# Optimization experiments

Hardware: AMD Instinct MI355X
Metric: run time of the kernel (lower is better)

Reference implementation:

```python
import jax, jax.numpy as jnp
import numpy as np

LOOPS = 2
NUM_GROUPS = 4
EXPERTS_PER_GROUP = 2
NUM_EXPERTS = NUM_GROUPS * EXPERTS_PER_GROUP
GROUPS_TOP_K = 2
TOP_K = 1
RMS_EPS = 1e-6
EPS = 1e-9


def setup_inputs() -> dict:
    key = jax.random.key(0)
    ks = jax.random.split(key, 6)
    B, S, D, F = 2, 1024, 1024, 2048
    return {
        "z": jax.random.normal(ks[0], (B, S, D), jnp.float32),
        "norm_w": jnp.ones((D,), jnp.float32),
        "w_macro": jax.random.normal(ks[1], (NUM_GROUPS, D), jnp.float32) * (D ** -0.5),
        "w_micro": jax.random.normal(ks[2], (NUM_GROUPS, EXPERTS_PER_GROUP, D), jnp.float32) * (D ** -0.5),
        "w1": jax.random.normal(ks[3], (NUM_EXPERTS, F, D), jnp.float32) * (D ** -0.5),
        "w2": jax.random.normal(ks[4], (NUM_EXPERTS, D, F), jnp.float32) * (F ** -0.5),
    }


def _rmsnorm(x, w):
    return x * jax.lax.rsqrt(jnp.mean(x * x, axis=-1, keepdims=True) + RMS_EPS) * w


def _combine_weights(x_flat, w_macro, w_micro):
    """Dense [T, E] combine matrix equivalent to the sort-based dispatch."""
    T = x_flat.shape[0]
    macro = jax.nn.softmax(x_flat @ w_macro.T, axis=-1)                    # [T, G]
    mvals, midx = jax.lax.top_k(macro, GROUPS_TOP_K)                       # [T, Gk]
    mvals = mvals / (jnp.sum(mvals, axis=-1, keepdims=True) + EPS)
    micro = jax.nn.softmax(jnp.einsum('td,ged->tge', x_flat, w_micro), axis=-1)  # [T, G, Eg]
    uvals, uidx = jax.lax.top_k(micro, TOP_K)                              # [T, G, k]
    uvals = uvals / (jnp.sum(uvals, axis=-1, keepdims=True) + EPS)
    tok = jnp.arange(T)
    combine = jnp.zeros((T, NUM_EXPERTS), x_flat.dtype)
    for s in range(GROUPS_TOP_K):
        g = midx[:, s]                                                     # [T]
        wg = mvals[:, s:s + 1]                                             # [T, 1]
        li = uidx[tok, g]                                                  # [T, k] local expert ids in group g
        lv = uvals[tok, g]                                                 # [T, k]
        eidx = g[:, None] * EXPERTS_PER_GROUP + li                         # [T, k] global expert ids
        combine = combine.at[tok[:, None], eidx].add(lv * wg)
    return combine


def reference(z, norm_w, w_macro, w_micro, w1, w2):
    B, S, D = z.shape
    T = B * S
    for _ in range(LOOPS):
        zn = _rmsnorm(z, norm_w)
        x = zn.reshape(T, D)
        combine = _combine_weights(x, w_macro, w_micro)                    # [T, E]
        # Dense equivalent of gather -> per-expert FFN -> weighted index_add
        h = jax.nn.silu(jnp.einsum('td,efd->tef', x, w1))                  # [T, E, F]
        y = jnp.einsum('tef,edf->ted', h, w2)                              # [T, E, D]
        mixed = jnp.einsum('ted,te->td', y, combine)                       # [T, D]
        z = z + mixed.reshape(B, S, D)
    return z
```

## Files before the change

kernel.cpp:

```cpp
#include <hip/hip_runtime.h>
#include <cstdint>
#include <cstddef>

#define T_TOK 2048
#define DDIM  1024
#define FDIM  2048

typedef __attribute__((ext_vector_type(8))) short bf16x8;
typedef __attribute__((ext_vector_type(4))) float f32x4;

static __device__ __forceinline__ float b2f(unsigned short u) {
  union { unsigned int i; float f; } v; v.i = ((unsigned int)u) << 16; return v.f;
}
static __device__ __forceinline__ unsigned short f2b(float f) {
  unsigned int x = __float_as_uint(f);
  return (unsigned short)((x + 0x7fffu + ((x >> 16) & 1u)) >> 16);
}
static __device__ __forceinline__ unsigned int pack2(float a, float b) {
  return (unsigned int)f2b(a) | ((unsigned int)f2b(b) << 16);
}
static __device__ __forceinline__ void gload_lds16(const void* g, void* l) {
  __builtin_amdgcn_global_load_lds(
      (const __attribute__((address_space(1))) void*)g,
      (__attribute__((address_space(3))) void*)l, 16, 0, 0);
}

__global__ void k_probe(const unsigned int* __restrict__ nw, int* __restrict__ flag) {
  if (threadIdx.x == 0) flag[0] = (nw[0] == 0x3F800000u) ? 0 : 1;
}

__global__ void k_init(const void* __restrict__ zin, float* __restrict__ z32,
                       const int* __restrict__ flag) {
  const int i = blockIdx.x * blockDim.x + threadIdx.x;
  float4 f;
  if (flag[0]) {
    ushort4 u = ((const ushort4*)zin)[i];
    f.x = b2f(u.x); f.y = b2f(u.y); f.z = b2f(u.z); f.w = b2f(u.w);
  } else {
    f = ((const float4*)zin)[i];
  }
  ((float4*)z32)[i] = f;
}

__global__ void k_out(const float* __restrict__ z32, void* __restrict__ out,
                      const int* __restrict__ flag) {
  const int i = blockIdx.x * blockDim.x + threadIdx.x;
  const float4 a = ((const float4*)z32)[i];
  if (flag[0]) {
    ushort4 o; o.x = f2b(a.x); o.y = f2b(a.y); o.z = f2b(a.z); o.w = f2b(a.w);
    ((ushort4*)out)[i] = o;
  } else {
    ((float4*)out)[i] = a;
  }
}

__global__ void k_split(const float* __restrict__ w, unsigned short* __restrict__ hi,
                        unsigned short* __restrict__ lo, const int* __restrict__ flag) {
  if (flag[0]) return;
  const size_t i = (size_t)blockIdx.x * blockDim.x + threadIdx.x;
  const float4 v = ((const float4*)w)[i];
  ushort4 h, l;
  h.x = f2b(v.x); l.x = f2b(v.x - b2f(h.x));
  h.y = f2b(v.y); l.y = f2b(v.y - b2f(h.y));
  h.z = f2b(v.z); l.z = f2b(v.z - b2f(h.z));
  h.w = f2b(v.w); l.w = f2b(v.w - b2f(h.w));
  ((ushort4*)hi)[i] = h;
  ((ushort4*)lo)[i] = l;
}

__global__ void k_rms_route(const float* __restrict__ z32,
                            const void* __restrict__ nw,
                            const void* __restrict__ wmac,
                            const void* __restrict__ wmic,
                            const int* __restrict__ flag,
                            unsigned short* __restrict__ xh,
                            unsigned short* __restrict__ xl,
                            float* __restrict__ logits,
                            const int base)
{
  const int tl = blockIdx.x;
  const int t  = base + tl;
  const int tid = threadIdx.x;
  const int lane = tid & 63, wv = tid >> 6;
  const int isbf = flag[0];
  const float4 zv = ((const float4*)(z32 + (size_t)t * DDIM))[tid];
  float ss = zv.x*zv.x + zv.y*zv.y + zv.z*zv.z + zv.w*zv.w;
  #pragma unroll
  for (int o = 32; o > 0; o >>= 1) ss += __shfl_down(ss, o);
  __shared__ float red[4];
  __shared__ float lred[12][4];
  if (lane == 0) red[wv] = ss;
  __syncthreads();
  const float tot = red[0] + red[1] + red[2] + red[3];
  const float scale = 1.f / sqrtf(tot * (1.f / DDIM) + 1e-6f);
  float4 nwv;
  if (isbf) {
    ushort4 u = ((const ushort4*)nw)[tid];
    nwv.x = b2f(u.x); nwv.y = b2f(u.y); nwv.z = b2f(u.z); nwv.w = b2f(u.w);
  } else {
    nwv = ((const float4*)nw)[tid];
  }
  float4 xn;
  xn.x = zv.x * scale * nwv.x;
  xn.y = zv.y * scale * nwv.y;
  xn.z = zv.z * scale * nwv.z;
  xn.w = zv.w * scale * nwv.w;
  ushort4 h4, l4;
  h4.x = f2b(xn.x); l4.x = f2b(xn.x - b2f(h4.x));
  h4.y = f2b(xn.y); l4.y = f2b(xn.y - b2f(h4.y));
  h4.z = f2b(xn.z); l4.z = f2b(xn.z - b2f(h4.z));
  h4.w = f2b(xn.w); l4.w = f2b(xn.w - b2f(h4.w));
  ((ushort4*)(xh + (size_t)tl * DDIM))[tid] = h4;
  ((ushort4*)(xl + (size_t)tl * DDIM))[tid] = l4;

  float part[12];
  #pragma unroll
  for (int r = 0; r < 4; r++) {
    float4 w;
    if (isbf) {
      ushort4 u = ((const ushort4*)wmac)[r * 256 + tid];
      w.x = b2f(u.x); w.y = b2f(u.y); w.z = b2f(u.z); w.w = b2f(u.w);
    } else {
      w = ((const float4*)wmac)[r * 256 + tid];
    }
    part[r] = xn.x*w.x + xn.y*w.y + xn.z*w.z + xn.w*w.w;
  }
  #pragma unroll
  for (int r = 0; r < 8; r++) {
    float4 w;
    if (isbf) {
      ushort4 u = ((const ushort4*)wmic)[r * 256 + tid];
      w.x = b2f(u.x); w.y = b2f(u.y); w.z = b2f(u.z); w.w = b2f(u.w);
    } else {
      w = ((const float4*)wmic)[r * 256 + tid];
    }
    part[4 + r] = xn.x*w.x + xn.y*w.y + xn.z*w.z + xn.w*w.w;
  }
  #pragma unroll
  for (int r = 0; r < 12; r++) {
    float v = part[r];
    #pragma unroll
    for (int o = 32; o > 0; o >>= 1) v += __shfl_down(v, o);
    if (lane == 0) lred[r][wv] = v;
  }
  __syncthreads();
  if (tid < 12)
    logits[tl * 12 + tid] = lred[tid][0] + lred[tid][1] + lred[tid][2] + lred[tid][3];
}

__global__ void k_route_a(const float* __restrict__ logits, int* __restrict__ eidx,
                          float* __restrict__ cw, int* __restrict__ counts, const int Tc)
{
  const int t = blockIdx.x * 256 + threadIdx.x;
  if (t >= Tc) return;
  const float* lg = logits + t * 12;
  float p[4];
  float m = fmaxf(fmaxf(lg[0], lg[1]), fmaxf(lg[2], lg[3]));
  float s = 0.f;
  #pragma unroll
  for (int i = 0; i < 4; i++) { p[i] = expf(lg[i] - m); s += p[i]; }
  #pragma unroll
  for (int i = 0; i < 4; i++) p[i] /= s;
  int i1 = 0;
  #pragma unroll
  for (int i = 1; i < 4; i++) if (p[i] > p[i1]) i1 = i;
  int i2 = (i1 == 0) ? 1 : 0;
  #pragma unroll
  for (int i = 0; i < 4; i++) if (i != i1 && p[i] > p[i2]) i2 = i;
  const float denom = p[i1] + p[i2] + 1e-9f;
  const int gs[2] = { i1, i2 };
  #pragma unroll
  for (int sI = 0; sI < 2; sI++) {
    const int g = gs[sI];
    const float wg = p[g] / denom;
    const float u0 = lg[4 + 2*g], u1 = lg[4 + 2*g + 1];
    const int li = (u1 > u0) ? 1 : 0;
    const float uval = 1.f / (1.f + expf(-fabsf(u0 - u1)));
    const float lv = uval / (uval + 1e-9f);
    const int e = g * 2 + li;
    eidx[t*2 + sI] = e;
    cw[t*2 + sI] = wg * lv;
    atomicAdd(&counts[e], 1);
  }
}

__global__ void k_route_b(const int* __restrict__ counts, int* __restrict__ offsets) {
  if (threadIdx.x == 0) {
    int o = 0;
    for (int e = 0; e < 8; e++) { offsets[e] = o; o += counts[e]; }
    offsets[8] = o;
  }
}

__global__ void k_route_c(const int* __restrict__ eidx, const float* __restrict__ cw,
                          const int* __restrict__ offsets, int* __restrict__ counts2,
                          int* __restrict__ tok, float* __restrict__ wof, const int Tc)
{
  const int t = blockIdx.x * 256 + threadIdx.x;
  if (t >= Tc) return;
  #pragma unroll
  for (int sI = 0; sI < 2; sI++) {
    const int e = eidx[t*2 + sI];
    const int pos = atomicAdd(&counts2[e], 1);
    const int a = offsets[e] + pos;
    tok[a] = t;
    wof[a] = cw[t*2 + sI];
  }
}

template<int KDIM, bool IS_G1, int KSPLIT>
__launch_bounds__(256)
__global__ void k_gemm(const unsigned short* __restrict__ Ah,
                       const unsigned short* __restrict__ Al,
                       const void* __restrict__ Bw,
                       const unsigned short* __restrict__ Bh_pre,
                       const unsigned short* __restrict__ Bl_pre,
                       const int* __restrict__ flag,
                       const int presplit,
                       const int* __restrict__ offsets,
                       const int* __restrict__ tok_of_a,
                       const float* __restrict__ w_of_a,
                       unsigned short* __restrict__ hh_out,
                       unsigned short* __restrict__ hl_out,
                       float* __restrict__ z32,
                       const int Nsize, const int base)
{
  const int e = blockIdx.z / KSPLIT;
  const int kpart = blockIdx.z - e * KSPLIT;
  const int offs = offsets[e];
  const int n_e = offsets[e + 1] - offs;
  const int rbase = blockIdx.y * 128;
  if (rbase >= n_e) return;
  const int cbase = blockIdx.x * 128;
  const int isbf = flag[0];

  __shared__ __align__(16) unsigned short Ahs[128 * 64];
  __shared__ __align__(16) unsigned short Als[128 * 64];
  __shared__ __align__(16) unsigned short Bhs[128 * 64];
  __shared__ __align__(16) unsigned short Bls[128 * 64];

  const int tid = threadIdx.x;
  const int lane = tid & 63;
  const int wv = tid >> 6;
  const int wr = (wv >> 1) * 64;
  const int wc = (wv & 1) * 64;
  const int lr = lane & 15;
  const int quad = lane >> 4;

  size_t aoff[4], boff[4];
  int gsw[4], loff[4];
  const int ch = tid & 7;
  #pragma unroll
  for (int c = 0; c < 4; c++) {
    const int row = c * 32 + (tid >> 3);
    int rl = rbase + row; if (rl > n_e - 1) rl = n_e - 1;
    if constexpr (IS_G1) aoff[c] = (size_t)tok_of_a[offs + rl] * KDIM;
    else                 aoff[c] = (size_t)(offs + rl) * KDIM;
    boff[c] = ((size_t)e * Nsize + cbase + row) * (size_t)KDIM;
    gsw[c]  = (ch ^ (row & 7)) * 8;
    loff[c] = row * 64 + gsw[c];
  }
  int lbase[4];
  #pragma unroll
  for (int c = 0; c < 4; c++) lbase[c] = (c * 32 + wv * 8) * 64;

  f32x4 acc[4][4];
  #pragma unroll
  for (int mt = 0; mt < 4; mt++)
    #pragma unroll
    for (int nt = 0; nt < 4; nt++)
      acc[mt][nt] = (f32x4){0.f, 0.f, 0.f, 0.f};

  const int KCH = KDIM / KSPLIT;
  const int k_lo = kpart * KCH;
  for (int k0 = k_lo; k0 < k_lo + KCH; k0 += 64) {
    __syncthreads();
    #pragma unroll
    for (int c = 0; c < 4; c++) {
      gload_lds16(Ah + aoff[c] + k0 + gsw[c], &Ahs[lbase[c]]);
      gload_lds16(Al + aoff[c] + k0 + gsw[c], &Als[lbase[c]]);
    }
    if (isbf) {
      const unsigned short* B16 = (const unsigned short*)Bw;
      #pragma unroll
      for (int c = 0; c < 4; c++)
        gload_lds16(B16 + boff[c] + k0 + gsw[c], &Bhs[lbase[c]]);
    } else if (presplit) {
      #pragma unroll
      for (int c = 0; c < 4; c++) {
        gload_lds16(Bh_pre + boff[c] + k0 + gsw[c], &Bhs[lbase[c]]);
        gload_lds16(Bl_pre + boff[c] + k0 + gsw[c], &Bls[lbase[c]]);
      }
    } else {
      const float* B32 = (const float*)Bw;
      #pragma unroll
      for (int c = 0; c < 4; c++) {
        const float* bsrc = B32 + boff[c] + k0 + (ch * 8);
        const float4 v0 = *(const float4*)(bsrc);
        const float4 v1 = *(const float4*)(bsrc + 4);
        uint4 bh, bl;
        bh.x = pack2(v0.x, v0.y); bh.y = pack2(v0.z, v0.w);
        bh.z = pack2(v1.x, v1.y); bh.w = pack2(v1.z, v1.w);
        bl.x = pack2(v0.x - b2f((unsigned short)(bh.x & 0xFFFF)), v0.y - b2f((unsigned short)(bh.x >> 16)));
        bl.y = pack2(v0.z - b2f((unsigned short)(bh.y & 0xFFFF)), v0.w - b2f((unsigned short)(bh.y >> 16)));
        bl.z = pack2(v1.x - b2f((unsigned short)(bh.z & 0xFFFF)), v1.y - b2f((unsigned short)(bh.z >> 16)));
        bl.w = pack2(v1.z - b2f((unsigned short)(bh.w & 0xFFFF)), v1.w - b2f((unsigned short)(bh.w >> 16)));
        *(uint4*)(&Bhs[loff[c]]) = bh;
        *(uint4*)(&Bls[loff[c]]) = bl;
      }
    }
    __syncthreads();
    #pragma unroll
    for (int ks = 0; ks < 2; ks++) {
      const int swz = ((ks * 4 + quad) ^ (lr & 7)) * 8;
      bf16x8 af[4], alf[4], bhf[4];
      #pragma unroll
      for (int mt = 0; mt < 4; mt++) {
        const int r = wr + mt * 16 + lr;
        af[mt]  = *(const bf16x8*)(&Ahs[r * 64 + swz]);
        alf[mt] = *(const bf16x8*)(&Als[r * 64 + swz]);
      }
      #pragma unroll
      for (int nt = 0; nt < 4; nt++) {
        const int r = wc + nt * 16 + lr;
        bhf[nt] = *(const bf16x8*)(&Bhs[r * 64 + swz]);
      }
      if (isbf) {
        #pragma unroll
        for (int mt = 0; mt < 4; mt++)
          #pragma unroll
          for (int nt = 0; nt < 4; nt++) {
            acc[mt][nt] = __builtin_amdgcn_mfma_f32_16x16x32_bf16(af[mt],  bhf[nt], acc[mt][nt], 0, 0, 0);
            acc[mt][nt] = __builtin_amdgcn_mfma_f32_16x16x32_bf16(alf[mt], bhf[nt], acc[mt][nt], 0, 0, 0);
          }
      } else {
        bf16x8 blf[4];
        #pragma unroll
        for (int nt = 0; nt < 4; nt++) {
          const int r = wc + nt * 16 + lr;
          blf[nt] = *(const bf16x8*)(&Bls[r * 64 + swz]);
        }
        #pragma unroll
        for (int mt = 0; mt < 4; mt++)
          #pragma unroll
          for (int nt = 0; nt < 4; nt++) {
            acc[mt][nt] = __builtin_amdgcn_mfma_f32_16x16x32_bf16(af[mt],  bhf[nt], acc[mt][nt], 0, 0, 0);
            acc[mt][nt] = __builtin_amdgcn_mfma_f32_16x16x32_bf16(alf[mt], bhf[nt], acc[mt][nt], 0, 0, 0);
            acc[mt][nt] = __builtin_amdgcn_mfma_f32_16x16x32_bf16(af[mt],  blf[nt], acc[mt][nt], 0, 0, 0);
          }
      }
    }
  }

  #pragma unroll
  for (int mt = 0; mt < 4; mt++) {
    #pragma unroll
    for (int reg = 0; reg < 4; reg++) {
      const int rl = rbase + wr + mt * 16 + quad * 4 + reg;
      if (rl < n_e) {
        if constexpr (IS_G1) {
          const size_t ro = (size_t)(offs + rl) * Nsize;
          #pragma unroll
          for (int nt = 0; nt < 4; nt++) {
            const int col = cbase + wc + nt * 16 + lr;
            const float v = acc[mt][nt][reg];
            const float sv = v / (1.f + expf(-v));
            const unsigned short hi = f2b(sv);
            hh_out[ro + col] = hi;
            hl_out[ro + col] = f2b(sv - b2f(hi));
          }
        } else {
          const float w = w_of_a[offs + rl];
          const size_t to = (size_t)(base + tok_of_a[offs + rl]) * Nsize;
          #pragma unroll
          for (int nt = 0; nt < 4; nt++) {
            const int col = cbase + wc + nt * 16 + lr;
            atomicAdd(&z32[to + col], acc[mt][nt][reg] * w);
          }
        }
      }
    }
  }
}

extern "C" void kernel_launch(void* const* d_in, const int* in_sizes, int n_in,
                              void* d_out, int out_size, void* d_ws, size_t ws_size,
                              hipStream_t stream)
{
  (void)in_sizes; (void)n_in; (void)out_size;
  const void* z_in = d_in[0];
  const void* nw   = d_in[1];
  const void* wmac = d_in[2];
  const void* wmic = d_in[3];
  const void* w1   = d_in[4];
  const void* w2   = d_in[5];

  auto rup = [](size_t x) -> size_t { return (x + 255) & ~(size_t)255; };
  auto need = [&](int c) -> size_t {
    size_t Tc = T_TOK / c;
    size_t s = 0;
    s += rup(4);
    s += rup((size_t)T_TOK * DDIM * 4);
    s += rup(Tc * DDIM * 2) * 2;
    s += rup(Tc * 12 * 4);
    s += rup(Tc * 2 * 4) * 2;
    s += 256 + 256;
    s += rup(2 * Tc * 4) * 2;
    s += rup(2 * Tc * (size_t)FDIM * 2) * 2;
    return s;
  };
  const size_t WELEM = (size_t)8 * FDIM * DDIM;
  const size_t wsplit_total = WELEM * 2 * 4;

  int presplit = 0;
  int C;
  if (need(1) + wsplit_total <= ws_size) { C = 1; presplit = 1; }
  else if (need(1) <= ws_size) C = 1;
  else if (need(2) <= ws_size) C = 2;
  else if (need(4) <= ws_size) C = 4;
  else C = 8;
  const int Tc = T_TOK / C;

  char* ws = (char*)d_ws;
  size_t off = 0;
  auto alloc = [&](size_t bytes) -> void* {
    void* p = ws + off;
    off += rup(bytes);
    return p;
  };
  int* flag            = (int*)alloc(4);
  float* z32           = (float*)alloc((size_t)T_TOK * DDIM * 4);
  unsigned short* xh   = (unsigned short*)alloc((size_t)Tc * DDIM * 2);
  unsigned short* xl   = (unsigned short*)alloc((size_t)Tc * DDIM * 2);
  float* logits        = (float*)alloc((size_t)Tc * 12 * 4);
  int* eidx            = (int*)alloc((size_t)Tc * 2 * 4);
  float* cw            = (float*)alloc((size_t)Tc * 2 * 4);
  int* counts          = (int*)alloc(64);
  int* offsets         = (int*)alloc(64);
  int* tok             = (int*)alloc((size_t)2 * Tc * 4);
  float* wof           = (float*)alloc((size_t)2 * Tc * 4);
  unsigned short* hh   = (unsigned short*)alloc((size_t)2 * Tc * FDIM * 2);
  unsigned short* hl   = (unsigned short*)alloc((size_t)2 * Tc * FDIM * 2);
  unsigned short *w1h = nullptr, *w1l = nullptr, *w2h = nullptr, *w2l = nullptr;
  if (presplit) {
    w1h = (unsigned short*)alloc(WELEM * 2);
    w1l = (unsigned short*)alloc(WELEM * 2);
    w2h = (unsigned short*)alloc(WELEM * 2);
    w2l = (unsigned short*)alloc(WELEM * 2);
  }

  k_probe<<<1, 64, 0, stream>>>((const unsigned int*)nw, flag);
  k_init<<<T_TOK * DDIM / 1024, 256, 0, stream>>>(z_in, z32, flag);
  if (presplit) {
    const int sb = (int)(WELEM / 4 / 256);
    k_split<<<sb, 256, 0, stream>>>((const float*)w1, w1h, w1l, flag);
    k_split<<<sb, 256, 0, stream>>>((const float*)w2, w2h, w2l, flag);
  }
  for (int L = 0; L < 2; L++) {
    for (int cb = 0; cb < C; cb++) {
      const int base = cb * Tc;
      hipMemsetAsync(counts, 0, 64, stream);
      k_rms_route<<<Tc, 256, 0, stream>>>(z32, nw, wmac, wmic, flag, xh, xl, logits, base);
      k_route_a<<<Tc / 256, 256, 0, stream>>>(logits, eidx, cw, counts, Tc);
      k_route_b<<<1, 64, 0, stream>>>(counts, offsets);
      k_route_c<<<Tc / 256, 256, 0, stream>>>(eidx, cw, offsets, counts + 8, tok, wof, Tc);
      k_gemm<DDIM, true, 1><<<dim3(FDIM / 128, Tc / 128, 8), 256, 0, stream>>>(
          xh, xl, w1, w1h, w1l, flag, presplit, offsets, tok, nullptr, hh, hl, nullptr, FDIM, base);
      k_gemm<FDIM, false, 2><<<dim3(DDIM / 128, Tc / 128, 16), 256, 0, stream>>>(
          hh, hl, w2, w2h, w2l, flag, presplit, offsets, tok, wof, nullptr, nullptr, z32, DDIM, base);
    }
  }
  k_out<<<T_TOK * DDIM / 1024, 256, 0, stream>>>(z32, d_out, flag);
}
```

Before: 613.2 us.

## Double-buffer GEMM K tiles and remap workgroups across XCDs for weight reuse

The grouped expert GEMM kernel now stages 32-wide K slices into two LDS buffers, so global-to-LDS loads for the next slice overlap MFMA work on the current one. This replaces the single-buffered 64-wide tile that synchronised around every load. Workgroup IDs are also remapped: the grid puts the token-row blocks on x, and each block is assigned through an XCD-aware interleave so that blocks sharing the same weight columns land on the same chiplet's L2. The LDS swizzle is reworked for the narrower 32-element rows. Costs are an extra barrier per 32-K step and a more complex index mapping, and early-exit blocks may now be spread unevenly across CUs.

```diff
diff --git a/kernel.cpp b/kernel.cpp
--- a/kernel.cpp
+++ b/kernel.cpp
@@ -208,6 +208,84 @@
   }
 }
 
+#define STAGE_ALL(B, K0) do {                                                      \
+    if (isbf) {                                                                    \
+      const unsigned short* B16 = (const unsigned short*)Bw;                       \
+      _Pragma("unroll")                                                            \
+      for (int c = 0; c < 2; c++) {                                                \
+        gload_lds16(Ah + aoff2[c] + (K0) + gsw,  &Ahs[B][lbase2[c]]);              \
+        gload_lds16(Al + aoff2[c] + (K0) + gsw,  &Als[B][lbase2[c]]);              \
+        gload_lds16(B16 + boff2[c] + (K0) + gsw, &Bhs[B][lbase2[c]]);              \
+      }                                                                            \
+    } else if (presplit) {                                                         \
+      _Pragma("unroll")                                                            \
+      for (int c = 0; c < 2; c++) {                                                \
+        gload_lds16(Ah + aoff2[c] + (K0) + gsw,     &Ahs[B][lbase2[c]]);           \
+        gload_lds16(Al + aoff2[c] + (K0) + gsw,     &Als[B][lbase2[c]]);           \
+        gload_lds16(Bh_pre + boff2[c] + (K0) + gsw, &Bhs[B][lbase2[c]]);           \
+        gload_lds16(Bl_pre + boff2[c] + (K0) + gsw, &Bls[B][lbase2[c]]);           \
+      }                                                                            \
+    } else {                                                                       \
+      const float* B32 = (const float*)Bw;                                         \
+      _Pragma("unroll")                                                            \
+      for (int c = 0; c < 2; c++) {                                                \
+        gload_lds16(Ah + aoff2[c] + (K0) + gsw, &Ahs[B][lbase2[c]]);               \
+        gload_lds16(Al + aoff2[c] + (K0) + gsw, &Als[B][lbase2[c]]);               \
+        const float* bsrc = B32 + boff2[c] + (K0) + ch2 * 8;                       \
+        const float4 v0 = *(const float4*)(bsrc);                                  \
+        const float4 v1 = *(const float4*)(bsrc + 4);                              \
+        uint4 bh, bl;                                                              \
+        bh.x = pack2(v0.x, v0.y); bh.y = pack2(v0.z, v0.w);                        \
+        bh.z = pack2(v1.x, v1.y); bh.w = pack2(v1.z, v1.w);                        \
+        bl.x = pack2(v0.x - b2f((unsigned short)(bh.x & 0xFFFF)), v0.y - b2f((unsigned short)(bh.x >> 16))); \
+        bl.y = pack2(v0.z - b2f((unsigned short)(bh.y & 0xFFFF)), v0.w - b2f((unsigned short)(bh.y >> 16))); \
+        bl.z = pack2(v1.x - b2f((unsigned short)(bh.z & 0xFFFF)), v1.y - b2f((unsigned short)(bh.z >> 16))); \
+        bl.w = pack2(v1.z - b2f((unsigned short)(bh.w & 0xFFFF)), v1.w - b2f((unsigned short)(bh.w >> 16))); \
+        *(uint4*)(&Bhs[B][loff2[c]]) = bh;                                         \
+        *(uint4*)(&Bls[B][loff2[c]]) = bl;                                         \
+      }                                                                            \
+    }                                                                              \
+  } while (0)
+
+#define COMPUTE(B) do {                                                            \
+    bf16x8 af[4], alf[4], bhf[4];                                                  \
+    _Pragma("unroll")                                                              \
+    for (int mt = 0; mt < 4; mt++) {                                               \
+      const int r = wr + mt * 16 + lr;                                             \
+      af[mt]  = *(const bf16x8*)(&Ahs[B][r * 32 + rsl]);                           \
+      alf[mt] = *(const bf16x8*)(&Als[B][r * 32 + rsl]);                           \
+    }                                                                              \
+    _Pragma("unroll")                                                              \
+    for (int nt = 0; nt < 4; nt++) {                                               \
+      const int r = wc + nt * 16 + lr;                                             \
+      bhf[nt] = *(const bf16x8*)(&Bhs[B][r * 32 + rsl]);                           \
+    }                                                                              \
+    if (isbf) {                                                                    \
+      _Pragma("unroll")                                                            \
+      for (int mt = 0; mt < 4; mt++)                                               \
+        _Pragma("unroll")                                                          \
+        for (int nt = 0; nt < 4; nt++) {                                           \
+          acc[mt][nt] = __builtin_amdgcn_mfma_f32_16x16x32_bf16(af[mt],  bhf[nt], acc[mt][nt], 0, 0, 0); \
+          acc[mt][nt] = __builtin_amdgcn_mfma_f32_16x16x32_bf16(alf[mt], bhf[nt], acc[mt][nt], 0, 0, 0); \
+        }                                                                          \
+    } else {                                                                       \
+      bf16x8 blf[4];                                                               \
+      _Pragma("unroll")                                                            \
+      for (int nt = 0; nt < 4; nt++) {                                             \
+        const int r = wc + nt * 16 + lr;                                           \
+        blf[nt] = *(const bf16x8*)(&Bls[B][r * 32 + rsl]);                         \
+      }                                                                            \
+      _Pragma("unroll")                                                            \
+      for (int mt = 0; mt < 4; mt++)                                               \
+        _Pragma("unroll")                                                          \
+        for (int nt = 0; nt < 4; nt++) {                                           \
+          acc[mt][nt] = __builtin_amdgcn_mfma_f32_16x16x32_bf16(af[mt],  bhf[nt], acc[mt][nt], 0, 0, 0); \
+          acc[mt][nt] = __builtin_amdgcn_mfma_f32_16x16x32_bf16(alf[mt], bhf[nt], acc[mt][nt], 0, 0, 0); \
+          acc[mt][nt] = __builtin_amdgcn_mfma_f32_16x16x32_bf16(af[mt],  blf[nt], acc[mt][nt], 0, 0, 0); \
+        }                                                                          \
+    }                                                                              \
+  } while (0)
+
 template<int KDIM, bool IS_G1, int KSPLIT>
 __launch_bounds__(256)
 __global__ void k_gemm(const unsigned short* __restrict__ Ah,
@@ -225,19 +303,28 @@
                        float* __restrict__ z32,
                        const int Nsize, const int base)
 {
-  const int e = blockIdx.z / KSPLIT;
-  const int kpart = blockIdx.z - e * KSPLIT;
+  const int gx = gridDim.x, gy = gridDim.y;
+  const int nwg = gx * gy * gridDim.z;
+  const int bid = blockIdx.x + gx * (blockIdx.y + gy * blockIdx.z);
+  const int virt = (bid & 7) * (nwg >> 3) + (bid >> 3);
+  const int rblk = virt % gx;
+  const int rest = virt / gx;
+  const int cblk = rest % gy;
+  const int ez   = rest / gy;
+  const int e = ez / KSPLIT;
+  const int kpart = ez % KSPLIT;
+
   const int offs = offsets[e];
   const int n_e = offsets[e + 1] - offs;
-  const int rbase = blockIdx.y * 128;
+  const int rbase = rblk * 128;
   if (rbase >= n_e) return;
-  const int cbase = blockIdx.x * 128;
+  const int cbase = cblk * 128;
   const int isbf = flag[0];
 
-  __shared__ __align__(16) unsigned short Ahs[128 * 64];
-  __shared__ __align__(16) unsigned short Als[128 * 64];
-  __shared__ __align__(16) unsigned short Bhs[128 * 64];
-  __shared__ __align__(16) unsigned short Bls[128 * 64];
+  __shared__ __align__(16) unsigned short Ahs[2][128 * 32];
+  __shared__ __align__(16) unsigned short Als[2][128 * 32];
+  __shared__ __align__(16) unsigned short Bhs[2][128 * 32];
+  __shared__ __align__(16) unsigned short Bls[2][128 * 32];
 
   const int tid = threadIdx.x;
   const int lane = tid & 63;
@@ -247,22 +334,21 @@
   const int lr = lane & 15;
   const int quad = lane >> 4;
 
-  size_t aoff[4], boff[4];
-  int gsw[4], loff[4];
-  const int ch = tid & 7;
-  #pragma unroll
-  for (int c = 0; c < 4; c++) {
-    const int row = c * 32 + (tid >> 3);
+  const int ch2 = tid & 3;
+  const int gsw = ((ch2 ^ ((tid >> 3) & 3)) * 8);
+  size_t aoff2[2], boff2[2];
+  int loff2[2], lbase2[2];
+  #pragma unroll
+  for (int c = 0; c < 2; c++) {
+    const int row = c * 64 + (tid >> 2);
     int rl = rbase + row; if (rl > n_e - 1) rl = n_e - 1;
-    if constexpr (IS_G1) aoff[c] = (size_t)tok_of_a[offs + rl] * KDIM;
-    else                 aoff[c] = (size_t)(offs + rl) * KDIM;
-    boff[c] = ((size_t)e * Nsize + cbase + row) * (size_t)KDIM;
-    gsw[c]  = (ch ^ (row & 7)) * 8;
-    loff[c] = row * 64 + gsw[c];
-  }
-  int lbase[4];
-  #pragma unroll
-  for (int c = 0; c < 4; c++) lbase[c] = (c * 32 + wv * 8) * 64;
+    if constexpr (IS_G1) aoff2[c] = (size_t)tok_of_a[offs + rl] * KDIM;
+    else                 aoff2[c] = (size_t)(offs + rl) * KDIM;
+    boff2[c] = ((size_t)e * Nsize + cbase + row) * (size_t)KDIM;
+    loff2[c] = row * 32 + gsw;
+    lbase2[c] = (c * 64 + wv * 16) * 32;
+  }
+  const int rsl = (quad ^ ((lr >> 1) & 3)) * 8;
 
   f32x4 acc[4][4];
   #pragma unroll
@@ -273,83 +359,17 @@
 
   const int KCH = KDIM / KSPLIT;
   const int k_lo = kpart * KCH;
-  for (int k0 = k_lo; k0 < k_lo + KCH; k0 += 64) {
+  const int k_hi = k_lo + KCH;
+
+  STAGE_ALL(0, k_lo);
+  __syncthreads();
+  for (int k0 = k_lo; k0 < k_hi; k0 += 64) {
+    STAGE_ALL(1, k0 + 32);
+    COMPUTE(0);
     __syncthreads();
-    #pragma unroll
-    for (int c = 0; c < 4; c++) {
-      gload_lds16(Ah + aoff[c] + k0 + gsw[c], &Ahs[lbase[c]]);
-      gload_lds16(Al + aoff[c] + k0 + gsw[c], &Als[lbase[c]]);
-    }
-    if (isbf) {
-      const unsigned short* B16 = (const unsigned short*)Bw;
-      #pragma unroll
-      for (int c = 0; c < 4; c++)
-        gload_lds16(B16 + boff[c] + k0 + gsw[c], &Bhs[lbase[c]]);
-    } else if (presplit) {
-      #pragma unroll
-      for (int c = 0; c < 4; c++) {
-        gload_lds16(Bh_pre + boff[c] + k0 + gsw[c], &Bhs[lbase[c]]);
-        gload_lds16(Bl_pre + boff[c] + k0 + gsw[c], &Bls[lbase[c]]);
-      }
-    } else {
-      const float* B32 = (const float*)Bw;
-      #pragma unroll
-      for (int c = 0; c < 4; c++) {
-        const float* bsrc = B32 + boff[c] + k0 + (ch * 8);
-        const float4 v0 = *(const float4*)(bsrc);
-        const float4 v1 = *(const float4*)(bsrc + 4);
-        uint4 bh, bl;
-        bh.x = pack2(v0.x, v0.y); bh.y = pack2(v0.z, v0.w);
-        bh.z = pack2(v1.x, v1.y); bh.w = pack2(v1.z, v1.w);
-        bl.x = pack2(v0.x - b2f((unsigned short)(bh.x & 0xFFFF)), v0.y - b2f((unsigned short)(bh.x >> 16)));
-        bl.y = pack2(v0.z - b2f((unsigned short)(bh.y & 0xFFFF)), v0.w - b2f((unsigned short)(bh.y >> 16)));
-        bl.z = pack2(v1.x - b2f((unsigned short)(bh.z & 0xFFFF)), v1.y - b2f((unsigned short)(bh.z >> 16)));
-        bl.w = pack2(v1.z - b2f((unsigned short)(bh.w & 0xFFFF)), v1.w - b2f((unsigned short)(bh.w >> 16)));
-        *(uint4*)(&Bhs[loff[c]]) = bh;
-        *(uint4*)(&Bls[loff[c]]) = bl;
-      }
-    }
+    if (k0 + 64 < k_hi) STAGE_ALL(0, k0 + 64);
+    COMPUTE(1);
     __syncthreads();
-    #pragma unroll
-    for (int ks = 0; ks < 2; ks++) {
-      const int swz = ((ks * 4 + quad) ^ (lr & 7)) * 8;
-      bf16x8 af[4], alf[4], bhf[4];
-      #pragma unroll
-      for (int mt = 0; mt < 4; mt++) {
-        const int r = wr + mt * 16 + lr;
-        af[mt]  = *(const bf16x8*)(&Ahs[r * 64 + swz]);
-        alf[mt] = *(const bf16x8*)(&Als[r * 64 + swz]);
-      }
-      #pragma unroll
-      for (int nt = 0; nt < 4; nt++) {
-        const int r = wc + nt * 16 + lr;
-        bhf[nt] = *(const bf16x8*)(&Bhs[r * 64 + swz]);
-      }
-      if (isbf) {
-        #pragma unroll
-        for (int mt = 0; mt < 4; mt++)
-          #pragma unroll
-          for (int nt = 0; nt < 4; nt++) {
-            acc[mt][nt] = __builtin_amdgcn_mfma_f32_16x16x32_bf16(af[mt],  bhf[nt], acc[mt][nt], 0, 0, 0);
-            acc[mt][nt] = __builtin_amdgcn_mfma_f32_16x16x32_bf16(alf[mt], bhf[nt], acc[mt][nt], 0, 0, 0);
-          }
-      } else {
-        bf16x8 blf[4];
-        #pragma unroll
-        for (int nt = 0; nt < 4; nt++) {
-          const int r = wc + nt * 16 + lr;
-          blf[nt] = *(const bf16x8*)(&Bls[r * 64 + swz]);
-        }
-        #pragma unroll
-        for (int mt = 0; mt < 4; mt++)
-          #pragma unroll
-          for (int nt = 0; nt < 4; nt++) {
-            acc[mt][nt] = __builtin_amdgcn_mfma_f32_16x16x32_bf16(af[mt],  bhf[nt], acc[mt][nt], 0, 0, 0);
-            acc[mt][nt] = __builtin_amdgcn_mfma_f32_16x16x32_bf16(alf[mt], bhf[nt], acc[mt][nt], 0, 0, 0);
-            acc[mt][nt] = __builtin_amdgcn_mfma_f32_16x16x32_bf16(af[mt],  blf[nt], acc[mt][nt], 0, 0, 0);
-          }
-      }
-    }
   }
 
   #pragma unroll
@@ -383,6 +403,9 @@
   }
 }
 
+#undef STAGE_ALL
+#undef COMPUTE
+
 extern "C" void kernel_launch(void* const* d_in, const int* in_sizes, int n_in,
                               void* d_out, int out_size, void* d_ws, size_t ws_size,
                               hipStream_t stream)
@@ -464,9 +487,9 @@
       k_route_a<<<Tc / 256, 256, 0, stream>>>(logits, eidx, cw, counts, Tc);
       k_route_b<<<1, 64, 0, stream>>>(counts, offsets);
       k_route_c<<<Tc / 256, 256, 0, stream>>>(eidx, cw, offsets, counts + 8, tok, wof, Tc);
-      k_gemm<DDIM, true, 1><<<dim3(FDIM / 128, Tc / 128, 8), 256, 0, stream>>>(
+      k_gemm<DDIM, true, 1><<<dim3(Tc / 128, FDIM / 128, 8), 256, 0, stream>>>(
           xh, xl, w1, w1h, w1l, flag, presplit, offsets, tok, nullptr, hh, hl, nullptr, FDIM, base);
-      k_gemm<FDIM, false, 2><<<dim3(DDIM / 128, Tc / 128, 16), 256, 0, stream>>>(
+      k_gemm<FDIM, false, 2><<<dim3(Tc / 128, DDIM / 128, 16), 256, 0, stream>>>(
           hh, hl, w2, w2h, w2l, flag, presplit, offsets, tok, wof, nullptr, nullptr, z32, DDIM, base);
     }
   }
```

After: 657.8 us. +7.3%, slower.
